# Performance work log

Measured on AMD Instinct MI355X. Metric: run time of the kernel, lower is better.

## Reference

```python
import jax, jax.numpy as jnp
from jax import lax
import numpy as np

B, CIN, COUT, N, H, W = 16, 64, 64, 8, 128, 128


def setup_inputs() -> dict:
    key = jax.random.key(0)
    ks = jax.random.split(key, 6)
    s = 0.05
    return {
        "x": jax.random.normal(ks[0], (B, CIN, H, W), dtype=jnp.float32),
        "condition": jax.random.normal(ks[1], (B, CIN), dtype=jnp.float32),
        "filt_w": jax.random.normal(ks[2], (N, COUT, CIN, 3, 3), dtype=jnp.float32) * s,
        "filt_b": jax.random.normal(ks[3], (N, COUT), dtype=jnp.float32) * s,
        "sel_w": jax.random.normal(ks[4], (N, CIN), dtype=jnp.float32) * s,
        "sel_b": jax.random.normal(ks[5], (N,), dtype=jnp.float32) * s,
    }


def reference(x, condition, filt_w, filt_b, sel_w, sel_b):
    b = x.shape[0]
    # condition selector: Linear(in_channels -> num_conditions) + softmax
    logits = condition.reshape(b, -1) @ sel_w.T + sel_b          # [B, N]
    weights = jax.nn.softmax(logits, axis=-1)                    # [B, N]

    n, cout, cin, kh, kw = filt_w.shape
    # Run all N branch convs in ONE conv by stacking filters on the output-channel axis.
    kern = filt_w.reshape(n * cout, cin, kh, kw)
    y = lax.conv_general_dilated(
        x, kern, window_strides=(1, 1), padding="SAME",
        dimension_numbers=("NCHW", "OIHW", "NCHW"))              # [B, N*COUT, H, W]
    h, w = y.shape[-2], y.shape[-1]
    y = y.reshape(b, n, cout, h, w) + filt_b.reshape(1, n, cout, 1, 1)
    # softmax-gated sum over the N branches
    out = jnp.einsum("bn,bnohw->bohw", weights, y)
    return out
```

## Files before the change

kernel.cpp:

```cpp
#include <hip/hip_runtime.h>
#include <stdint.h>

#define BATCH 16
#define CIN   64
#define COUT  64
#define NBR   8
#define HH    128
#define WW    128

typedef __attribute__((ext_vector_type(8)))  short short8;
typedef __attribute__((ext_vector_type(16))) float f32x16;

__device__ __forceinline__ unsigned int f2bf_hi(float f) {
    union { float f; uint32_t u; } v; v.f = f;
    return (v.u + 0x8000u) >> 16;
}
__device__ __forceinline__ unsigned short f2bf(float f) {
    union { float f; uint32_t u; } v; v.f = f;
    uint32_t u = v.u;
    return (unsigned short)((u + 0x7FFFu + ((u >> 16) & 1u)) >> 16);
}
__device__ __forceinline__ short8 gld_frag(const unsigned short* p) {
    union { uint4 u; short8 s; } t;
    t.u = *(const uint4*)p;
    return t.s;
}
__device__ __forceinline__ short8 lds_frag(const unsigned short* p) {
    union { uint2 u[2]; short8 s; } t;
    t.u[0] = *(const uint2*)p;
    t.u[1] = *(const uint2*)(p + 4);
    return t.s;
}

__global__ __launch_bounds__(256)
void k_prep(const float* __restrict__ cond,
            const float* __restrict__ sel_w,
            const float* __restrict__ sel_b,
            const float* __restrict__ filt_w,
            const float* __restrict__ filt_b,
            unsigned short* __restrict__ wfilt,
            float* __restrict__ cbias) {
    __shared__ float4 lw4[NBR * 144];
    __shared__ float lg[NBR];
    float* lw = (float*)lw4;

    const int blk = blockIdx.x;
    const int b = blk >> 6, o = blk & 63;
    const int tid = threadIdx.x;

    const float4* src4 = (const float4*)filt_w;
    #pragma unroll
    for (int i = tid; i < NBR * 144; i += 256)
        lw4[i] = src4[((i / 144) * COUT + o) * 144 + (i % 144)];

    {
        const int lane = tid & 63, w = tid >> 6;
        const float c0 = cond[b * CIN + lane];
        #pragma unroll
        for (int k = 0; k < 2; ++k) {
            const int n = w + k * 4;
            float p = c0 * sel_w[n * CIN + lane];
            #pragma unroll
            for (int off = 32; off > 0; off >>= 1)
                p += __shfl_down(p, off, 64);
            if (lane == 0) lg[n] = p + sel_b[n];
        }
    }
    __syncthreads();

    float w8[NBR];
    {
        float m = -1e30f;
        #pragma unroll
        for (int n = 0; n < NBR; ++n) m = fmaxf(m, lg[n]);
        float s = 0.f;
        #pragma unroll
        for (int n = 0; n < NBR; ++n) { w8[n] = __expf(lg[n] - m); s += w8[n]; }
        const float inv = 1.f / s;
        #pragma unroll
        for (int n = 0; n < NBR; ++n) w8[n] *= inv;
    }

    #pragma unroll
    for (int idx = tid; idx < 576; idx += 256) {
        const int t = idx >> 6, c = idx & 63;
        float acc = 0.f;
        #pragma unroll
        for (int n = 0; n < NBR; ++n)
            acc += w8[n] * lw[n * 576 + c * 9 + t];
        wfilt[(((long)(b * 9 + t) * COUT + o) << 6) + c] = f2bf(acc);
    }
    if (tid == 0) {
        float ab = 0.f;
        #pragma unroll
        for (int n = 0; n < NBR; ++n) ab += w8[n] * filt_b[n * COUT + o];
        cbias[b * COUT + o] = ab;
    }
}

#define RT 8
#define WT 32
#define SLABW 34
#define SLABR 10
#define PSTR  68

__global__ __launch_bounds__(256, 2)
void k_conv4(const float* __restrict__ x,
             const unsigned short* __restrict__ wfilt,
             const float* __restrict__ cbias,
             float* __restrict__ out) {
    __shared__ unsigned short lx[SLABR * SLABW * PSTR];

    const int b  = blockIdx.z;
    const int h0 = blockIdx.y * RT;
    const int w0 = blockIdx.x * WT;
    const int tid = threadIdx.x;

    for (int task = tid; task < SLABR * 32 * 10; task += 256) {
        const int j  = task % 10;
        const int r  = task / 10;
        const int cp = r & 31;
        const int s  = r >> 5;
        const int c  = cp * 2;
        const int hin   = h0 + s - 1;
        const int wbase = w0 - 4 + j * 4;
        float4 v0, v1;
        v0.x = v0.y = v0.z = v0.w = 0.f;
        v1 = v0;
        if (hin >= 0 && hin < HH && wbase >= 0 && wbase < WW) {
            const float* px = x + (((long)(b * CIN + c) * HH + hin) * WW + wbase);
            v0 = *(const float4*)px;
            v1 = *(const float4*)(px + (long)HH * WW);
        }
        unsigned int d[4];
        d[0] = f2bf_hi(v0.x) | (f2bf_hi(v1.x) << 16);
        d[1] = f2bf_hi(v0.y) | (f2bf_hi(v1.y) << 16);
        d[2] = f2bf_hi(v0.z) | (f2bf_hi(v1.z) << 16);
        d[3] = f2bf_hi(v0.w) | (f2bf_hi(v1.w) << 16);
        #pragma unroll
        for (int i = 0; i < 4; ++i) {
            const int p = j * 4 - 3 + i;
            if (p >= 0 && p < SLABW)
                *(unsigned int*)&lx[(s * SLABW + p) * PSTR + c] = d[i];
        }
    }

    const int lane = tid & 63;
    const int wave = tid >> 6;
    const int l31  = lane & 31;
    const int lh   = lane >> 5;
    const int r0   = wave * 2;

    const unsigned short* wf = wfilt + (long)b * 9 * COUT * CIN;

    short8 A0[4], A1[4];
    #pragma unroll
    for (int cc = 0; cc < 4; ++cc) {
        A0[cc] = gld_frag(wf + l31 * CIN + cc * 16 + lh * 8);
        A1[cc] = gld_frag(wf + (32 + l31) * CIN + cc * 16 + lh * 8);
    }

    f32x16 acc00, acc01, acc10, acc11;
    #pragma unroll
    for (int i = 0; i < 16; ++i) {
        const int m = (i & 3) + 8 * (i >> 2) + 4 * lh;
        const float b0 = cbias[b * COUT + m];
        const float b1 = cbias[b * COUT + 32 + m];
        acc00[i] = b0; acc01[i] = b0;
        acc10[i] = b1; acc11[i] = b1;
    }

    __syncthreads();

    #pragma unroll
    for (int tap = 0; tap < 9; ++tap) {
        short8 nA0[4], nA1[4];
        if (tap < 8) {
            const unsigned short* wn = wf + (long)(tap + 1) * COUT * CIN;
            #pragma unroll
            for (int cc = 0; cc < 4; ++cc) {
                nA0[cc] = gld_frag(wn + l31 * CIN + cc * 16 + lh * 8);
                nA1[cc] = gld_frag(wn + (32 + l31) * CIN + cc * 16 + lh * 8);
            }
        }
        const int kh = tap / 3, kw = tap % 3;
        #pragma unroll
        for (int cc = 0; cc < 4; ++cc) {
            const int kofs = cc * 16 + lh * 8;
            short8 b0 = lds_frag(&lx[((r0     + kh) * SLABW + l31 + kw) * PSTR + kofs]);
            short8 b1 = lds_frag(&lx[((r0 + 1 + kh) * SLABW + l31 + kw) * PSTR + kofs]);
            acc00 = __builtin_amdgcn_mfma_f32_32x32x16_bf16(A0[cc], b0, acc00, 0, 0, 0);
            acc01 = __builtin_amdgcn_mfma_f32_32x32x16_bf16(A0[cc], b1, acc01, 0, 0, 0);
            acc10 = __builtin_amdgcn_mfma_f32_32x32x16_bf16(A1[cc], b0, acc10, 0, 0, 0);
            acc11 = __builtin_amdgcn_mfma_f32_32x32x16_bf16(A1[cc], b1, acc11, 0, 0, 0);
        }
        #pragma unroll
        for (int cc = 0; cc < 4; ++cc) { A0[cc] = nA0[cc]; A1[cc] = nA1[cc]; }
    }

    #pragma unroll
    for (int cb = 0; cb < 2; ++cb) {
        #pragma unroll
        for (int pb = 0; pb < 2; ++pb) {
            const f32x16 v = cb == 0 ? (pb == 0 ? acc00 : acc01)
                                     : (pb == 0 ? acc10 : acc11);
            const int hrow = h0 + r0 + pb;
            float* op = out + (((long)(b * COUT + cb * 32) * HH + hrow) * WW + w0 + l31);
            #pragma unroll
            for (int i = 0; i < 16; ++i) {
                const int m = (i & 3) + 8 * (i >> 2) + 4 * lh;
                op[(long)m * HH * WW] = v[i];
            }
        }
    }
}

extern "C" void kernel_launch(void* const* d_in, const int* in_sizes, int n_in,
                              void* d_out, int out_size, void* d_ws, size_t ws_size,
                              hipStream_t stream) {
    const float* x      = (const float*)d_in[0];
    const float* cond   = (const float*)d_in[1];
    const float* filt_w = (const float*)d_in[2];
    const float* filt_b = (const float*)d_in[3];
    const float* sel_w  = (const float*)d_in[4];
    const float* sel_b  = (const float*)d_in[5];
    float* out = (float*)d_out;

    float*          cbias = (float*)d_ws;
    unsigned short* wfilt = (unsigned short*)((char*)d_ws + 4096);

    k_prep<<<BATCH * COUT, 256, 0, stream>>>(cond, sel_w, sel_b, filt_w, filt_b, wfilt, cbias);

    dim3 grid(WW / WT, HH / RT, BATCH);
    k_conv4<<<grid, 256, 0, stream>>>(x, wfilt, cbias, out);
}
```

Baseline: 178.3 us.

## Pre-cast input to padded channels-last bf16 buffer before conv

Adds a separate kernel that converts the fp32 NCHW input into a zero-padded NHWC bf16 workspace buffer. The conv kernel then fills its LDS slab with plain 16-byte vector loads, with no bounds checks, no conversion and no transposition, and reads half the bytes it read before. The cost is an extra kernel launch and an extra full pass over the input (read fp32, write bf16). The cast kernel's reads are strided across channels, so they may be poorly coalesced.

```diff
diff --git a/kernel.cpp b/kernel.cpp
--- a/kernel.cpp
+++ b/kernel.cpp
@@ -7,6 +7,8 @@
 #define NBR   8
 #define HH    128
 #define WW    128
+#define XBH   130
+#define XBW   130
 
 typedef __attribute__((ext_vector_type(8)))  short short8;
 typedef __attribute__((ext_vector_type(16))) float f32x16;
@@ -98,6 +100,30 @@
     }
 }
 
+__global__ __launch_bounds__(256)
+void k_cast(const float* __restrict__ x, unsigned short* __restrict__ xb) {
+    const int b   = blockIdx.y;
+    const int hp  = blockIdx.x;
+    const int tid = threadIdx.x;
+    unsigned short* dst = xb + ((long)(b * XBH + hp) * XBW) * 64;
+    const bool zrow = (hp == 0) || (hp == XBH - 1);
+    const int h = hp - 1;
+    const long cs = (long)HH * WW;
+
+    for (int t = tid; t < XBW * 8; t += 256) {
+        const int wp = t >> 3, q = t & 7;
+        uint4 v; v.x = v.y = v.z = v.w = 0u;
+        if (!zrow && wp != 0 && wp != XBW - 1) {
+            const float* px = x + (((long)(b * CIN + q * 8)) * HH + h) * WW + (wp - 1);
+            v.x = f2bf_hi(px[0])      | (f2bf_hi(px[cs])     << 16);
+            v.y = f2bf_hi(px[2 * cs]) | (f2bf_hi(px[3 * cs]) << 16);
+            v.z = f2bf_hi(px[4 * cs]) | (f2bf_hi(px[5 * cs]) << 16);
+            v.w = f2bf_hi(px[6 * cs]) | (f2bf_hi(px[7 * cs]) << 16);
+        }
+        *(uint4*)&dst[t * 8] = v;
+    }
+}
+
 #define RT 8
 #define WT 32
 #define SLABW 34
@@ -105,7 +131,7 @@
 #define PSTR  68
 
 __global__ __launch_bounds__(256, 2)
-void k_conv4(const float* __restrict__ x,
+void k_conv4(const unsigned short* __restrict__ xb,
              const unsigned short* __restrict__ wfilt,
              const float* __restrict__ cbias,
              float* __restrict__ out) {
@@ -116,33 +142,18 @@
     const int w0 = blockIdx.x * WT;
     const int tid = threadIdx.x;
 
-    for (int task = tid; task < SLABR * 32 * 10; task += 256) {
-        const int j  = task % 10;
-        const int r  = task / 10;
-        const int cp = r & 31;
-        const int s  = r >> 5;
-        const int c  = cp * 2;
-        const int hin   = h0 + s - 1;
-        const int wbase = w0 - 4 + j * 4;
-        float4 v0, v1;
-        v0.x = v0.y = v0.z = v0.w = 0.f;
-        v1 = v0;
-        if (hin >= 0 && hin < HH && wbase >= 0 && wbase < WW) {
-            const float* px = x + (((long)(b * CIN + c) * HH + hin) * WW + wbase);
-            v0 = *(const float4*)px;
-            v1 = *(const float4*)(px + (long)HH * WW);
-        }
-        unsigned int d[4];
-        d[0] = f2bf_hi(v0.x) | (f2bf_hi(v1.x) << 16);
-        d[1] = f2bf_hi(v0.y) | (f2bf_hi(v1.y) << 16);
-        d[2] = f2bf_hi(v0.z) | (f2bf_hi(v1.z) << 16);
-        d[3] = f2bf_hi(v0.w) | (f2bf_hi(v1.w) << 16);
-        #pragma unroll
-        for (int i = 0; i < 4; ++i) {
-            const int p = j * 4 - 3 + i;
-            if (p >= 0 && p < SLABW)
-                *(unsigned int*)&lx[(s * SLABW + p) * PSTR + c] = d[i];
-        }
+    const unsigned short* xbb = xb + (long)b * XBH * XBW * 64;
+    for (int t = tid; t < SLABR * SLABW * 8; t += 256) {
+        const int s = t / (SLABW * 8);
+        const int i = t - s * (SLABW * 8);
+        const int p = i >> 3;
+        const int q = i & 7;
+        const uint4 v = *(const uint4*)(xbb + (((h0 + s) * XBW + w0 + p) << 6) + (q << 3));
+        uint2 u0, u1;
+        u0.x = v.x; u0.y = v.y; u1.x = v.z; u1.y = v.w;
+        unsigned short* lp = &lx[(s * SLABW + p) * PSTR + (q << 3)];
+        *(uint2*)lp       = u0;
+        *(uint2*)(lp + 4) = u1;
     }
 
     const int lane = tid & 63;
@@ -228,9 +239,13 @@
 
     float*          cbias = (float*)d_ws;
     unsigned short* wfilt = (unsigned short*)((char*)d_ws + 4096);
+    unsigned short* xb    = (unsigned short*)((char*)d_ws + 4096 + 1179648);
 
     k_prep<<<BATCH * COUT, 256, 0, stream>>>(cond, sel_w, sel_b, filt_w, filt_b, wfilt, cbias);
 
+    dim3 cg(XBH, BATCH);
+    k_cast<<<cg, 256, 0, stream>>>(x, xb);
+
     dim3 grid(WW / WT, HH / RT, BATCH);
-    k_conv4<<<grid, 256, 0, stream>>>(x, wfilt, cbias, out);
-}
+    k_conv4<<<grid, 256, 0, stream>>>(xb, wfilt, cbias, out);
+}
```

Result: slower. 184.1 us (+3.3%).
